# Kernel tuning notes

Hardware: AMD Instinct MI355X
Metric: run time of the kernel (lower is better)

## Reference

```python
import jax, jax.numpy as jnp
import numpy as np

B, D, U1, U2 = 16384, 512, 512, 512
BN_EPS = 1e-3  # keras BatchNormalization default epsilon


def sparsemax(z):
    # z: [..., D]; standard sparsemax along last axis (Martins & Astudillo)
    d = z.shape[-1]
    z_sorted = -jnp.sort(-z, axis=-1)                      # descending
    z_cum = jnp.cumsum(z_sorted, axis=-1)
    k = jnp.arange(1, d + 1, dtype=z.dtype)
    support = (1.0 + k * z_sorted) > z_cum                 # [..., D] bool
    k_z = jnp.sum(support, axis=-1, keepdims=True)         # support size
    tau = (jnp.take_along_axis(z_cum, k_z.astype(jnp.int32) - 1, axis=-1) - 1.0) / k_z.astype(z.dtype)
    return jnp.maximum(z - tau, 0.0)


def setup_inputs() -> dict:
    key = jax.random.key(0)
    ks = jax.random.split(key, 8)
    x = jax.random.normal(ks[0], (B, D), dtype=jnp.float32)
    W1 = jax.random.normal(ks[1], (D, U1), dtype=jnp.float32) * 0.05
    b1 = jnp.zeros((U1,), jnp.float32)
    centers = jax.random.normal(ks[2], (U2, D), dtype=jnp.float32)      # paraboloid centers
    coefs = jax.random.normal(ks[3], (U2, D), dtype=jnp.float32) * 0.1  # paraboloid axis coefficients
    bn_gamma = jnp.ones((D,), jnp.float32)
    bn_beta = jnp.zeros((D,), jnp.float32)
    bn_mean = jnp.zeros((D,), jnp.float32)
    bn_var = jnp.ones((D,), jnp.float32)
    W_out = jax.random.normal(ks[4], (U1 + U2, D), dtype=jnp.float32) * 0.05
    b_out = jnp.zeros((D,), jnp.float32)
    w_add = jnp.array([0.5, 0.5], jnp.float32)  # WeightedAdd learnable scalars
    return {"x": x, "W1": W1, "b1": b1, "centers": centers, "coefs": coefs,
            "bn_gamma": bn_gamma, "bn_beta": bn_beta, "bn_mean": bn_mean, "bn_var": bn_var,
            "W_out": W_out, "b_out": b_out, "w_add": w_add}


def reference(x, W1, b1, centers, coefs, bn_gamma, bn_beta, bn_mean, bn_var, W_out, b_out, w_add):
    # Dense branch
    h1 = jax.nn.relu(x @ W1 + b1)                               # [B, U1]
    # BoundedParaboloids branch: BatchNorm (inference stats) then bounded paraboloids
    xb = (x - bn_mean) * jax.lax.rsqrt(bn_var + BN_EPS) * bn_gamma + bn_beta
    # q_j = sum_d (coefs[j,d] * (xb_d - centers[j,d]))^2, computed via GEMMs
    A = coefs * coefs                                            # [U2, D]
    q = (xb * xb) @ A.T - 2.0 * (xb @ (A * centers).T) + jnp.sum(A * centers * centers, axis=-1)
    h2 = jax.nn.relu(1.0 - q)                                    # [B, U2] bounded paraboloids
    # Output embedding: Dense(relu) on concat
    emb = jax.nn.relu(jnp.concatenate([h1, h2], axis=-1) @ W_out + b_out)  # [B, D]
    # WeightedAdd of (dropout-identity) inputs and embedding; dropout_rate=0 / inference
    pre = w_add[0] * x + w_add[1] * emb
    mask = sparsemax(pre)                                        # [B, D]
    return mask
```

## Files before the change

### kernel.cpp

```cpp
#include <hip/hip_runtime.h>
#include <math.h>

typedef float f4 __attribute__((ext_vector_type(4)));
typedef float f32x4 __attribute__((ext_vector_type(4)));
typedef __bf16 bf16x8 __attribute__((ext_vector_type(8)));
typedef unsigned short u16;
typedef u16 us8 __attribute__((ext_vector_type(8)));

#define BN_EPS 1e-3f

__device__ __forceinline__ u16 f2bf(float f) {
  unsigned u = __builtin_bit_cast(unsigned, f);
  unsigned r = u + 0x7fffu + ((u >> 16) & 1u);
  return (u16)(r >> 16);
}
__device__ __forceinline__ float bf2f(u16 h) {
  unsigned u = ((unsigned)h) << 16;
  return __builtin_bit_cast(float, u);
}

__global__ __launch_bounds__(256) void prep_all_kernel(
    const float* __restrict__ x, const float* __restrict__ W1,
    const float* __restrict__ b1, const float* __restrict__ centers,
    const float* __restrict__ coefs, const float* __restrict__ gamma,
    const float* __restrict__ beta, const float* __restrict__ mean,
    const float* __restrict__ var, const float* __restrict__ W_out,
    u16* __restrict__ Xb, u16* __restrict__ Xsq, u16* __restrict__ Pth,
    float* __restrict__ cvec, u16* __restrict__ W1th, u16* __restrict__ Wth,
    float* __restrict__ b1a) {
  __shared__ float tsh[32][33];
  __shared__ float red[4][64];
  const int bid = blockIdx.x;
  const int tid = threadIdx.x;

  if (bid < 4096) {
    int gid = bid * 256 + tid;
    int m = gid >> 6;
    int d0 = (gid & 63) * 8;
    f4 v0 = *(const f4*)(x + (size_t)m * 512 + d0);
    f4 v1 = *(const f4*)(x + (size_t)m * 512 + d0 + 4);
    f4 g0 = *(const f4*)(gamma + d0);
    f4 g1 = *(const f4*)(gamma + d0 + 4);
    f4 be0 = *(const f4*)(beta + d0);
    f4 be1 = *(const f4*)(beta + d0 + 4);
    f4 mn0 = *(const f4*)(mean + d0);
    f4 mn1 = *(const f4*)(mean + d0 + 4);
    f4 va0 = *(const f4*)(var + d0);
    f4 va1 = *(const f4*)(var + d0 + 4);
    us8 ob, oq;
#pragma unroll
    for (int e = 0; e < 8; ++e) {
      float xv = (e < 4) ? v0[e] : v1[e - 4];
      float gv = (e < 4) ? g0[e] : g1[e - 4];
      float bv = (e < 4) ? be0[e] : be1[e - 4];
      float mv = (e < 4) ? mn0[e] : mn1[e - 4];
      float vv = (e < 4) ? va0[e] : va1[e - 4];
      float s = rsqrtf(vv + BN_EPS) * gv;
      float sh = bv - mv * s;
      float xbf = fmaf(xv, s, sh);
      ob[e] = f2bf(xbf);
      oq[e] = f2bf(xbf * xbf);
    }
    *(us8*)(Xb + (size_t)m * 512 + d0) = ob;
    *(us8*)(Xsq + (size_t)m * 512 + d0) = oq;
  } else if (bid < 4608) {
    int j = bid - 4096;
    int d = tid * 2;
    float acc = 0.f;
    u16 pa2[2], pb2[2];
#pragma unroll
    for (int e = 0; e < 2; ++e) {
      float cf = coefs[(size_t)j * 512 + d + e];
      float ce = centers[(size_t)j * 512 + d + e];
      float a = cf * cf;
      pa2[e] = f2bf(a);
      pb2[e] = f2bf(-2.f * a * ce);
      acc = fmaf(a * ce, ce, acc);
    }
    *(unsigned*)(Pth + (size_t)j * 1024 + d) =
        ((unsigned)pa2[1] << 16) | pa2[0];
    *(unsigned*)(Pth + (size_t)j * 1024 + 512 + d) =
        ((unsigned)pb2[1] << 16) | pb2[0];
#pragma unroll
    for (int off = 32; off; off >>= 1) acc += __shfl_xor(acc, off);
    if ((tid & 63) == 0) red[0][tid >> 6] = acc;
    __syncthreads();
    if (tid == 0)
      cvec[j] = red[0][0] + red[0][1] + red[0][2] + red[0][3];
  } else if (bid < 4864) {
    int i = bid - 4608;
    int lx = tid & 31, ly = tid >> 5;
    int n0 = (i & 15) * 32, k0 = (i >> 4) * 32;
#pragma unroll
    for (int q = 0; q < 4; ++q)
      tsh[ly + 8 * q][lx] = W1[(size_t)(k0 + ly + 8 * q) * 512 + n0 + lx];
    __syncthreads();
    int k = k0 + lx;
    float s = rsqrtf(var[k] + BN_EPS) * gamma[k];
#pragma unroll
    for (int q = 0; q < 4; ++q) {
      float v = tsh[lx][ly + 8 * q] / s;
      W1th[(size_t)(n0 + ly + 8 * q) * 512 + k] = f2bf(v);
    }
  } else if (bid < 5376) {
    int i = bid - 4864;
    int lx = tid & 31, ly = tid >> 5;
    int n0 = (i & 15) * 32, k0 = (i >> 4) * 32;
#pragma unroll
    for (int q = 0; q < 4; ++q)
      tsh[ly + 8 * q][lx] = W_out[(size_t)(k0 + ly + 8 * q) * 512 + n0 + lx];
    __syncthreads();
#pragma unroll
    for (int q = 0; q < 4; ++q) {
      float v = tsh[lx][ly + 8 * q];
      Wth[(size_t)(n0 + ly + 8 * q) * 1024 + k0 + lx] = f2bf(v);
    }
  } else {
    int b = bid - 5376;
    int lane = tid & 63;
    int kq = tid >> 6;
    int j = b * 64 + lane;
    float partial = 0.f;
    for (int i = 0; i < 128; ++i) {
      int k = kq * 128 + i;
      float s = rsqrtf(var[k] + BN_EPS) * gamma[k];
      float sh = beta[k] - mean[k] * s;
      partial = fmaf(sh, W1[(size_t)k * 512 + j] / s, partial);
    }
    red[kq][lane] = partial;
    __syncthreads();
    if (tid < 64) {
      float t = red[0][tid] + red[1][tid] + red[2][tid] + red[3][tid];
      b1a[b * 64 + tid] = b1[b * 64 + tid] - t;
    }
  }
}

__device__ __forceinline__ void wait_vm8() {
  asm volatile("s_waitcnt vmcnt(8)" ::: "memory");
}
__device__ __forceinline__ void wait_vm0() {
  asm volatile("s_waitcnt vmcnt(0)" ::: "memory");
}
__device__ __forceinline__ void sbar() { __builtin_amdgcn_s_barrier(); }
__device__ __forceinline__ void sgb0() { __builtin_amdgcn_sched_barrier(0); }

__global__ __launch_bounds__(256, 2) void gemm_fused12(
    const u16* __restrict__ Xb, const u16* __restrict__ Xsq,
    const u16* __restrict__ W1th, const u16* __restrict__ Pth,
    const float* __restrict__ b1a, const float* __restrict__ cvec,
    u16* __restrict__ Hout) {
  extern __shared__ char smem[];
  const int tid = threadIdx.x;
  const int l = tid & 63;
  const int w = tid >> 6;
  const int wm = w & 1, wn = w >> 1;
  const int lr = l & 15, lk = l >> 4;
  const int sx = lr & 7;
  const int bid = blockIdx.x;
  const int L = (bid & 7) * 128 + (bid >> 3);
  const int p = L >> 3;
  const int g = ((L >> 2) & 1) ^ 1;
  const int n = L & 3;
  const int m0 = p * 128, n0 = n * 128;
  const int Kg = g ? 1024 : 512;
  const int nt = g ? 16 : 8;
  const u16* Bmat = g ? Pth : W1th;
  const int srow = l >> 3;
  const int sslot = (l & 7) ^ srow;

  f32x4 acc[4][4];
#pragma unroll
  for (int i = 0; i < 4; ++i)
#pragma unroll
    for (int j = 0; j < 4; ++j) acc[i][j] = (f32x4){0.f, 0.f, 0.f, 0.f};

#define F12_STAGE(buf, k0)                                                    \
  {                                                                           \
    const u16* Asrc = g ? (((k0) < 512) ? Xsq : Xb) : Xb;                     \
    const int kb = (k0)&511;                                                  \
    char* dA = smem + (buf)*16384;                                            \
    char* dB = smem + 32768 + (buf)*16384;                                    \
    _Pragma("unroll") for (int pp = 0; pp < 4; ++pp) {                        \
      int c = pp * 4 + w;                                                     \
      int row = c * 8 + srow;                                                 \
      int loff = c * 1024;                                                    \
      size_t goa = (size_t)(m0 + row) * 512 + kb + sslot * 8;                 \
      size_t gob = (size_t)(n0 + row) * Kg + (k0) + sslot * 8;                \
      __builtin_amdgcn_global_load_lds(                                       \
          (const __attribute__((address_space(1))) void*)(Asrc + goa),        \
          (__attribute__((address_space(3))) void*)(dA + loff), 16, 0, 0);    \
      __builtin_amdgcn_global_load_lds(                                       \
          (const __attribute__((address_space(1))) void*)(Bmat + gob),        \
          (__attribute__((address_space(3))) void*)(dB + loff), 16, 0, 0);    \
    }                                                                         \
  }

  F12_STAGE(0, 0);
  F12_STAGE(1, 64);
  for (int t = 0; t < nt; ++t) {
    if (t + 1 < nt) {
      wait_vm8();
    } else {
      wait_vm0();
    }
    sgb0();
    sbar();
    sgb0();
    const char* sA = smem + (t & 1) * 16384;
    const char* sB = smem + 32768 + (t & 1) * 16384;
#pragma unroll
    for (int ks = 0; ks < 2; ++ks) {
      bf16x8 av[4], bv[4];
#pragma unroll
      for (int i = 0; i < 4; ++i)
        av[i] = *(const bf16x8*)(sA + (wm * 64 + i * 16 + lr) * 128 +
                                 (((ks * 4 + lk) ^ sx) * 16));
#pragma unroll
      for (int j = 0; j < 4; ++j)
        bv[j] = *(const bf16x8*)(sB + (wn * 64 + j * 16 + lr) * 128 +
                                 (((ks * 4 + lk) ^ sx) * 16));
#pragma unroll
      for (int i = 0; i < 4; ++i)
#pragma unroll
        for (int j = 0; j < 4; ++j)
          acc[i][j] = __builtin_amdgcn_mfma_f32_16x16x32_bf16(av[i], bv[j],
                                                              acc[i][j], 0, 0, 0);
    }
    sgb0();
    sbar();
    sgb0();
    if (t + 2 < nt) F12_STAGE(t & 1, (t + 2) * 64);
  }
#undef F12_STAGE

  const int mwb = m0 + wm * 64;
  const int nwb = n0 + wn * 64;
  const float* bias = g ? cvec : b1a;
#pragma unroll
  for (int j = 0; j < 4; ++j) {
    int nn = nwb + j * 16 + lr;
    float bv = bias[nn];
#pragma unroll
    for (int i = 0; i < 4; ++i) {
#pragma unroll
      for (int r = 0; r < 4; ++r) {
        int m = mwb + i * 16 + lk * 4 + r;
        float v = acc[i][j][r] + bv;
        v = g ? fmaxf(1.f - v, 0.f) : fmaxf(v, 0.f);
        Hout[(size_t)m * 1024 + g * 512 + nn] = f2bf(v);
      }
    }
  }
}

__global__ __launch_bounds__(256, 2) void gemm3(
    const u16* __restrict__ Ah, const u16* __restrict__ Bh,
    const float* __restrict__ bias, const float* __restrict__ xorig,
    const float* __restrict__ wadd, float* __restrict__ outp) {
  extern __shared__ char smem[];
  const int tid = threadIdx.x;
  const int l = tid & 63;
  const int w = tid >> 6;
  const int wm = w & 1, wn = w >> 1;
  const int lr = l & 15, lk = l >> 4;
  const int sx = lr & 7;
  const int bid = blockIdx.x;
  const int lin = (bid & 7) * 64 + (bid >> 3);
  const int m0 = (lin >> 2) * 128, n0 = (lin & 3) * 128;
  const int srow = l >> 3;
  const int sslot = (l & 7) ^ srow;

  f32x4 acc[4][4];
#pragma unroll
  for (int i = 0; i < 4; ++i)
#pragma unroll
    for (int j = 0; j < 4; ++j) acc[i][j] = (f32x4){0.f, 0.f, 0.f, 0.f};

#define G3_STAGE(buf, k0)                                                     \
  {                                                                           \
    char* dA = smem + (buf)*16384;                                            \
    char* dB = smem + 32768 + (buf)*16384;                                    \
    _Pragma("unroll") for (int pp = 0; pp < 4; ++pp) {                        \
      int c = pp * 4 + w;                                                     \
      int row = c * 8 + srow;                                                 \
      int loff = c * 1024;                                                    \
      size_t gob = (size_t)(n0 + row) * 1024 + (k0) + sslot * 8;              \
      size_t goa = (size_t)(m0 + row) * 1024 + (k0) + sslot * 8;              \
      __builtin_amdgcn_global_load_lds(                                       \
          (const __attribute__((address_space(1))) void*)(Bh + gob),          \
          (__attribute__((address_space(3))) void*)(dB + loff), 16, 0, 0);    \
      __builtin_amdgcn_global_load_lds(                                       \
          (const __attribute__((address_space(1))) void*)(Ah + goa),          \
          (__attribute__((address_space(3))) void*)(dA + loff), 16, 0, 0);    \
    }                                                                         \
  }

  G3_STAGE(0, 0);
  G3_STAGE(1, 64);
  for (int t = 0; t < 16; ++t) {
    if (t + 1 < 16) {
      wait_vm8();
    } else {
      wait_vm0();
    }
    sgb0();
    sbar();
    sgb0();
    const char* sA = smem + (t & 1) * 16384;
    const char* sB = smem + 32768 + (t & 1) * 16384;
#pragma unroll
    for (int ks = 0; ks < 2; ++ks) {
      bf16x8 av[4], bv[4];
#pragma unroll
      for (int i = 0; i < 4; ++i)
        av[i] = *(const bf16x8*)(sA + (wm * 64 + i * 16 + lr) * 128 +
                                 (((ks * 4 + lk) ^ sx) * 16));
#pragma unroll
      for (int j = 0; j < 4; ++j)
        bv[j] = *(const bf16x8*)(sB + (wn * 64 + j * 16 + lr) * 128 +
                                 (((ks * 4 + lk) ^ sx) * 16));
#pragma unroll
      for (int i = 0; i < 4; ++i)
#pragma unroll
        for (int j = 0; j < 4; ++j)
          acc[i][j] = __builtin_amdgcn_mfma_f32_16x16x32_bf16(av[i], bv[j],
                                                              acc[i][j], 0, 0, 0);
    }
    sgb0();
    sbar();
    sgb0();
    if (t + 2 < 16) G3_STAGE(t & 1, (t + 2) * 64);
  }
#undef G3_STAGE

  const int mwb = m0 + wm * 64;
  const int nwb = n0 + wn * 64;
  float w0 = wadd[0], w1 = wadd[1];
#pragma unroll
  for (int j = 0; j < 4; ++j) {
    int n = nwb + j * 16 + lr;
    float bv = bias[n];
#pragma unroll
    for (int i = 0; i < 4; ++i) {
#pragma unroll
      for (int r = 0; r < 4; ++r) {
        int m = mwb + i * 16 + lk * 4 + r;
        float v = fmaxf(acc[i][j][r] + bv, 0.f);
        outp[(size_t)m * 512 + n] = fmaf(w1, v, w0 * xorig[(size_t)m * 512 + n]);
      }
    }
  }
}

__global__ __launch_bounds__(256) void sparsemax_kernel(float* __restrict__ out) {
  int wrk = (blockIdx.x & 7) * 512 + (blockIdx.x >> 3);
  int row = wrk * 4 + (threadIdx.x >> 6);
  int lane = threadIdx.x & 63;
  float* rp = out + (size_t)row * 512;
  f4 z0 = *(const f4*)(rp + lane * 8);
  f4 z1 = *(const f4*)(rp + lane * 8 + 4);
  float z[8];
#pragma unroll
  for (int e = 0; e < 4; ++e) {
    z[e] = z0[e];
    z[4 + e] = z1[e];
  }
  float m = z[0];
#pragma unroll
  for (int i = 1; i < 8; ++i) m = fmaxf(m, z[i]);
#pragma unroll
  for (int off = 32; off; off >>= 1) m = fmaxf(m, __shfl_xor(m, off));
  float tau = m - 1.0f;
  for (int it = 0; it < 32; ++it) {
    float s = 0.f, k = 0.f;
#pragma unroll
    for (int i = 0; i < 8; ++i) {
      if (z[i] > tau) {
        s += z[i] - tau;
        k += 1.f;
      }
    }
#pragma unroll
    for (int off = 32; off; off >>= 1) {
      s += __shfl_xor(s, off);
      k += __shfl_xor(k, off);
    }
    if (k < 0.5f) break;
    float tn = tau + (s - 1.f) / k;
    if (tn == tau) break;
    tau = tn;
  }
  float s = 0.f, k = 0.f;
#pragma unroll
  for (int i = 0; i < 8; ++i)
    if (z[i] > tau) {
      s += z[i];
      k += 1.f;
    }
#pragma unroll
  for (int off = 32; off; off >>= 1) {
    s += __shfl_xor(s, off);
    k += __shfl_xor(k, off);
  }
  float tauf = (k >= 0.5f) ? (s - 1.f) / k : (m - 1.f);
  f4 o0, o1;
#pragma unroll
  for (int e = 0; e < 4; ++e) {
    o0[e] = fmaxf(z[e] - tauf, 0.f);
    o1[e] = fmaxf(z[4 + e] - tauf, 0.f);
  }
  *(f4*)(rp + lane * 8) = o0;
  *(f4*)(rp + lane * 8 + 4) = o1;
}

extern "C" void kernel_launch(void* const* d_in, const int* in_sizes, int n_in,
                              void* d_out, int out_size, void* d_ws,
                              size_t ws_size, hipStream_t stream) {
  const float* x = (const float*)d_in[0];
  const float* W1 = (const float*)d_in[1];
  const float* b1 = (const float*)d_in[2];
  const float* centers = (const float*)d_in[3];
  const float* coefs = (const float*)d_in[4];
  const float* gamma = (const float*)d_in[5];
  const float* beta = (const float*)d_in[6];
  const float* mean = (const float*)d_in[7];
  const float* var = (const float*)d_in[8];
  const float* W_out = (const float*)d_in[9];
  const float* b_out = (const float*)d_in[10];
  const float* wadd = (const float*)d_in[11];
  float* out = (float*)d_out;

  char* ws = (char*)d_ws;
  u16* Hh = (u16*)(ws);
  float* b1a = (float*)(ws + 33554432);
  u16* Wth = (u16*)(ws + 33562624);
  u16* Xb = (u16*)(ws + 50331648);
  char* pool = ws + 67108864;
  u16* W1th = (u16*)(pool);
  u16* Pth = (u16*)(pool + 1048576);
  float* cvec = (float*)(ws + 69206016);
  u16* Xsq = (u16*)d_out;

  prep_all_kernel<<<5384, 256, 0, stream>>>(x, W1, b1, centers, coefs, gamma,
                                            beta, mean, var, W_out, Xb, Xsq,
                                            Pth, cvec, W1th, Wth, b1a);

  gemm_fused12<<<1024, 256, 65536, stream>>>(Xb, Xsq, W1th, Pth, b1a, cvec,
                                             Hh);
  gemm3<<<512, 256, 65536, stream>>>(Hh, Wth, b_out, x, wadd, out);
  sparsemax_kernel<<<4096, 256, 0, stream>>>(out);
}
```

Measured before the change: 108.8 us.

## Fuse sparsemax into output GEMM with full-row tiles per block

```diff
diff --git a/kernel.cpp b/kernel.cpp
--- a/kernel.cpp
+++ b/kernel.cpp
@@ -138,6 +138,9 @@
 
 __device__ __forceinline__ void wait_vm8() {
   asm volatile("s_waitcnt vmcnt(8)" ::: "memory");
+}
+__device__ __forceinline__ void wait_vm9() {
+  asm volatile("s_waitcnt vmcnt(9)" ::: "memory");
 }
 __device__ __forceinline__ void wait_vm0() {
   asm volatile("s_waitcnt vmcnt(0)" ::: "memory");
@@ -254,20 +257,19 @@
   }
 }
 
-__global__ __launch_bounds__(256, 2) void gemm3(
+__global__ __launch_bounds__(512, 1) void gemm3_sm(
     const u16* __restrict__ Ah, const u16* __restrict__ Bh,
     const float* __restrict__ bias, const float* __restrict__ xorig,
     const float* __restrict__ wadd, float* __restrict__ outp) {
-  extern __shared__ char smem[];
+  __shared__ char smem[147456];
   const int tid = threadIdx.x;
   const int l = tid & 63;
   const int w = tid >> 6;
-  const int wm = w & 1, wn = w >> 1;
   const int lr = l & 15, lk = l >> 4;
   const int sx = lr & 7;
   const int bid = blockIdx.x;
-  const int lin = (bid & 7) * 64 + (bid >> 3);
-  const int m0 = (lin >> 2) * 128, n0 = (lin & 3) * 128;
+  const int q = (bid & 7) * 32 + (bid >> 3);
+  const int m0 = q * 64;
   const int srow = l >> 3;
   const int sslot = (l & 7) ^ srow;
 
@@ -277,48 +279,50 @@
 #pragma unroll
     for (int j = 0; j < 4; ++j) acc[i][j] = (f32x4){0.f, 0.f, 0.f, 0.f};
 
-#define G3_STAGE(buf, k0)                                                     \
+#define G3S_STAGE(buf, k0)                                                    \
   {                                                                           \
-    char* dA = smem + (buf)*16384;                                            \
-    char* dB = smem + 32768 + (buf)*16384;                                    \
-    _Pragma("unroll") for (int pp = 0; pp < 4; ++pp) {                        \
-      int c = pp * 4 + w;                                                     \
-      int row = c * 8 + srow;                                                 \
-      int loff = c * 1024;                                                    \
-      size_t gob = (size_t)(n0 + row) * 1024 + (k0) + sslot * 8;              \
+    char* dA = smem + (buf)*8192;                                             \
+    char* dB = smem + 16384 + (buf)*65536;                                    \
+    {                                                                         \
+      int row = w * 8 + srow;                                                 \
       size_t goa = (size_t)(m0 + row) * 1024 + (k0) + sslot * 8;              \
       __builtin_amdgcn_global_load_lds(                                       \
+          (const __attribute__((address_space(1))) void*)(Ah + goa),          \
+          (__attribute__((address_space(3))) void*)(dA + w * 1024), 16, 0, 0);\
+    }                                                                         \
+    _Pragma("unroll") for (int pp = 0; pp < 8; ++pp) {                        \
+      int c = pp * 8 + w;                                                     \
+      int row = c * 8 + srow;                                                 \
+      size_t gob = (size_t)row * 1024 + (k0) + sslot * 8;                     \
+      __builtin_amdgcn_global_load_lds(                                       \
           (const __attribute__((address_space(1))) void*)(Bh + gob),          \
-          (__attribute__((address_space(3))) void*)(dB + loff), 16, 0, 0);    \
-      __builtin_amdgcn_global_load_lds(                                       \
-          (const __attribute__((address_space(1))) void*)(Ah + goa),          \
-          (__attribute__((address_space(3))) void*)(dA + loff), 16, 0, 0);    \
+          (__attribute__((address_space(3))) void*)(dB + c * 1024), 16, 0, 0);\
     }                                                                         \
   }
 
-  G3_STAGE(0, 0);
-  G3_STAGE(1, 64);
+  G3S_STAGE(0, 0);
+  G3S_STAGE(1, 64);
   for (int t = 0; t < 16; ++t) {
     if (t + 1 < 16) {
-      wait_vm8();
+      wait_vm9();
     } else {
       wait_vm0();
     }
     sgb0();
     sbar();
     sgb0();
-    const char* sA = smem + (t & 1) * 16384;
-    const char* sB = smem + 32768 + (t & 1) * 16384;
+    const char* sA = smem + (t & 1) * 8192;
+    const char* sB = smem + 16384 + (t & 1) * 65536;
 #pragma unroll
     for (int ks = 0; ks < 2; ++ks) {
       bf16x8 av[4], bv[4];
 #pragma unroll
       for (int i = 0; i < 4; ++i)
-        av[i] = *(const bf16x8*)(sA + (wm * 64 + i * 16 + lr) * 128 +
+        av[i] = *(const bf16x8*)(sA + (i * 16 + lr) * 128 +
                                  (((ks * 4 + lk) ^ sx) * 16));
 #pragma unroll
       for (int j = 0; j < 4; ++j)
-        bv[j] = *(const bf16x8*)(sB + (wn * 64 + j * 16 + lr) * 128 +
+        bv[j] = *(const bf16x8*)(sB + (w * 64 + j * 16 + lr) * 128 +
                                  (((ks * 4 + lk) ^ sx) * 16));
 #pragma unroll
       for (int i = 0; i < 4; ++i)
@@ -330,88 +334,128 @@
     sgb0();
     sbar();
     sgb0();
-    if (t + 2 < 16) G3_STAGE(t & 1, (t + 2) * 64);
-  }
-#undef G3_STAGE
-
-  const int mwb = m0 + wm * 64;
-  const int nwb = n0 + wn * 64;
-  float w0 = wadd[0], w1 = wadd[1];
+    if (t + 2 < 16) G3S_STAGE(t & 1, (t + 2) * 64);
+  }
+#undef G3S_STAGE
+
+  __syncthreads();
+  float* mPart = (float*)smem;
+  float* sPart = (float*)(smem + 2048);
+  float* kPart = (float*)(smem + 4096);
+  float* tauLds = (float*)(smem + 6144);
+  const float w0 = wadd[0], w1 = wadd[1];
+
 #pragma unroll
   for (int j = 0; j < 4; ++j) {
-    int n = nwb + j * 16 + lr;
-    float bv = bias[n];
+    int col = w * 64 + j * 16 + lr;
+    float bv = bias[col];
 #pragma unroll
     for (int i = 0; i < 4; ++i) {
 #pragma unroll
       for (int r = 0; r < 4; ++r) {
-        int m = mwb + i * 16 + lk * 4 + r;
+        int m = m0 + i * 16 + lk * 4 + r;
         float v = fmaxf(acc[i][j][r] + bv, 0.f);
-        outp[(size_t)m * 512 + n] = fmaf(w1, v, w0 * xorig[(size_t)m * 512 + n]);
+        acc[i][j][r] = fmaf(w1, v, w0 * xorig[(size_t)m * 512 + col]);
       }
     }
   }
-}
-
-__global__ __launch_bounds__(256) void sparsemax_kernel(float* __restrict__ out) {
-  int wrk = (blockIdx.x & 7) * 512 + (blockIdx.x >> 3);
-  int row = wrk * 4 + (threadIdx.x >> 6);
-  int lane = threadIdx.x & 63;
-  float* rp = out + (size_t)row * 512;
-  f4 z0 = *(const f4*)(rp + lane * 8);
-  f4 z1 = *(const f4*)(rp + lane * 8 + 4);
-  float z[8];
-#pragma unroll
-  for (int e = 0; e < 4; ++e) {
-    z[e] = z0[e];
-    z[4 + e] = z1[e];
-  }
-  float m = z[0];
-#pragma unroll
-  for (int i = 1; i < 8; ++i) m = fmaxf(m, z[i]);
-#pragma unroll
-  for (int off = 32; off; off >>= 1) m = fmaxf(m, __shfl_xor(m, off));
-  float tau = m - 1.0f;
-  for (int it = 0; it < 32; ++it) {
-    float s = 0.f, k = 0.f;
-#pragma unroll
-    for (int i = 0; i < 8; ++i) {
-      if (z[i] > tau) {
-        s += z[i] - tau;
-        k += 1.f;
+  float mx[4][4];
+#pragma unroll
+  for (int i = 0; i < 4; ++i)
+#pragma unroll
+    for (int r = 0; r < 4; ++r) {
+      float m = acc[i][0][r];
+#pragma unroll
+      for (int j = 1; j < 4; ++j) m = fmaxf(m, acc[i][j][r]);
+      mx[i][r] = m;
+    }
+#pragma unroll
+  for (int off = 1; off < 16; off <<= 1)
+#pragma unroll
+    for (int i = 0; i < 4; ++i)
+#pragma unroll
+      for (int r = 0; r < 4; ++r)
+        mx[i][r] = fmaxf(mx[i][r], __shfl_xor(mx[i][r], off));
+  if (lr == 0) {
+#pragma unroll
+    for (int i = 0; i < 4; ++i)
+#pragma unroll
+      for (int r = 0; r < 4; ++r)
+        mPart[(i * 16 + lk * 4 + r) * 8 + w] = mx[i][r];
+  }
+  __syncthreads();
+  if (tid < 64) {
+    float m = mPart[tid * 8];
+#pragma unroll
+    for (int e = 1; e < 8; ++e) m = fmaxf(m, mPart[tid * 8 + e]);
+    tauLds[tid] = m - 1.0f;
+  }
+  __syncthreads();
+
+  for (int it = 0; it < 20; ++it) {
+    float sl[4][4], kl[4][4];
+#pragma unroll
+    for (int i = 0; i < 4; ++i)
+#pragma unroll
+      for (int r = 0; r < 4; ++r) {
+        float tau = tauLds[i * 16 + lk * 4 + r];
+        float s = 0.f, k = 0.f;
+#pragma unroll
+        for (int j = 0; j < 4; ++j) {
+          float v = acc[i][j][r];
+          if (v > tau) {
+            s += v;
+            k += 1.f;
+          }
+        }
+        sl[i][r] = s;
+        kl[i][r] = k;
       }
-    }
-#pragma unroll
-    for (int off = 32; off; off >>= 1) {
-      s += __shfl_xor(s, off);
-      k += __shfl_xor(k, off);
-    }
-    if (k < 0.5f) break;
-    float tn = tau + (s - 1.f) / k;
-    if (tn == tau) break;
-    tau = tn;
-  }
-  float s = 0.f, k = 0.f;
-#pragma unroll
-  for (int i = 0; i < 8; ++i)
-    if (z[i] > tau) {
-      s += z[i];
-      k += 1.f;
-    }
-#pragma unroll
-  for (int off = 32; off; off >>= 1) {
-    s += __shfl_xor(s, off);
-    k += __shfl_xor(k, off);
-  }
-  float tauf = (k >= 0.5f) ? (s - 1.f) / k : (m - 1.f);
-  f4 o0, o1;
-#pragma unroll
-  for (int e = 0; e < 4; ++e) {
-    o0[e] = fmaxf(z[e] - tauf, 0.f);
-    o1[e] = fmaxf(z[4 + e] - tauf, 0.f);
-  }
-  *(f4*)(rp + lane * 8) = o0;
-  *(f4*)(rp + lane * 8 + 4) = o1;
+#pragma unroll
+    for (int off = 1; off < 16; off <<= 1)
+#pragma unroll
+      for (int i = 0; i < 4; ++i)
+#pragma unroll
+        for (int r = 0; r < 4; ++r) {
+          sl[i][r] += __shfl_xor(sl[i][r], off);
+          kl[i][r] += __shfl_xor(kl[i][r], off);
+        }
+    if (lr == 0) {
+#pragma unroll
+      for (int i = 0; i < 4; ++i)
+#pragma unroll
+        for (int r = 0; r < 4; ++r) {
+          int row = i * 16 + lk * 4 + r;
+          sPart[row * 8 + w] = sl[i][r];
+          kPart[row * 8 + w] = kl[i][r];
+        }
+    }
+    __syncthreads();
+    if (tid < 64) {
+      float S = 0.f, K = 0.f;
+#pragma unroll
+      for (int e = 0; e < 8; ++e) {
+        S += sPart[tid * 8 + e];
+        K += kPart[tid * 8 + e];
+      }
+      tauLds[tid] = (S - 1.f) / K;
+    }
+    __syncthreads();
+  }
+
+#pragma unroll
+  for (int i = 0; i < 4; ++i)
+#pragma unroll
+    for (int r = 0; r < 4; ++r) {
+      int row = i * 16 + lk * 4 + r;
+      float tau = tauLds[row];
+      int m = m0 + row;
+#pragma unroll
+      for (int j = 0; j < 4; ++j) {
+        int col = w * 64 + j * 16 + lr;
+        outp[(size_t)m * 512 + col] = fmaxf(acc[i][j][r] - tau, 0.f);
+      }
+    }
 }
 
 extern "C" void kernel_launch(void* const* d_in, const int* in_sizes, int n_in,
@@ -448,6 +492,5 @@
 
   gemm_fused12<<<1024, 256, 65536, stream>>>(Xb, Xsq, W1th, Pth, b1a, cvec,
                                              Hh);
-  gemm3<<<512, 256, 65536, stream>>>(Hh, Wth, b_out, x, wadd, out);
-  sparsemax_kernel<<<4096, 256, 0, stream>>>(out);
-}
+  gemm3_sm<<<256, 512, 0, stream>>>(Hh, Wth, b_out, x, wadd, out);
+}
```

Result: slower. 175.8 us (+61.5%).
